# Kernel optimization log

Hardware: AMD Instinct MI355X
Metric: run time of the kernel (lower is better)

## Reference

```python
import jax, jax.numpy as jnp
import numpy as np
import math

N_NODES = 100000
N_EDGES = 3200000

_SQRT3 = math.sqrt(3.0)
_SQRT5 = math.sqrt(5.0)


def _spherical_harmonics_lmax2(v):
    """e3nn real spherical harmonics, lmax=2, normalize=True, normalization='component'.

    v: [E, 3] edge vectors (not necessarily unit).
    Returns [E, 9] = concat(Y0 [1], Y1 [3], Y2 [5]).
    """
    # normalize=True: evaluate SH on the unit vector
    u = v / jnp.linalg.norm(v, axis=1, keepdims=True)
    x, y, z = u[:, 0], u[:, 1], u[:, 2]
    # l=0 (component norm: *sqrt(1) = 1)
    sh0 = jnp.ones_like(x)
    # l=1 (component norm: *sqrt(3))
    sh1_0 = _SQRT3 * x
    sh1_1 = _SQRT3 * y
    sh1_2 = _SQRT3 * z
    # l=2 raw polynomials (norm-1 at unit vector), then *sqrt(5) for component norm
    x2, y2, z2 = x * x, y * y, z * z
    sh2_0 = _SQRT3 * x * z
    sh2_1 = _SQRT3 * x * y
    sh2_2 = y2 - 0.5 * (x2 + z2)
    sh2_3 = _SQRT3 * y * z
    sh2_4 = 0.5 * _SQRT3 * (z2 - x2)
    sh2 = _SQRT5 * jnp.stack([sh2_0, sh2_1, sh2_2, sh2_3, sh2_4], axis=-1)
    return jnp.concatenate(
        [sh0[:, None], jnp.stack([sh1_0, sh1_1, sh1_2], axis=-1), sh2], axis=-1
    )


def setup_inputs() -> dict:
    key = jax.random.key(0)
    k1, k2, k3 = jax.random.split(key, 3)
    pos = jax.random.normal(k1, (N_NODES, 3), dtype=jnp.float32)
    edge_index = jax.random.randint(k2, (2, N_EDGES), 0, N_NODES, dtype=jnp.int64)
    shift = jax.random.normal(k3, (N_EDGES, 3), dtype=jnp.float32)
    return {"pos": pos, "edge_index": edge_index, "shift": shift}


def reference(pos, edge_index, shift):
    # gather endpoints and form displacement vectors
    edge_vec = pos[edge_index[1]] - pos[edge_index[0]]  # [E, 3]
    edge_vec = edge_vec - shift
    edge_length = jnp.linalg.norm(edge_vec, axis=1)  # [E]
    edge_sh = _spherical_harmonics_lmax2(edge_vec)  # [E, 9]
    return (edge_vec, edge_length, edge_sh)
```

## Files before the change

### kernel.cpp

```cpp
#include <hip/hip_runtime.h>
#include <math.h>


#define SQRT3 1.7320508075688772f
#define SQRT5 2.2360679774997896f

typedef float v4f __attribute__((ext_vector_type(4)));

__global__ __launch_bounds__(256) void sh_edge_kernel(
    const float*  __restrict__ pos,
    const int*    __restrict__ edge_index,
    const float*  __restrict__ shift,
    float* __restrict__ out_vec,
    float* __restrict__ out_len,
    float* __restrict__ out_sh,
    int n_edges)
{
    __shared__ float s_shift[768];
    __shared__ float s_vec[768];
    __shared__ float s_sh[2304];

    const int tid  = threadIdx.x;
    const int base = blockIdx.x * 256;
    const int nblk = min(256, n_edges - base);
    const bool full = (nblk == 256);

    float psx = 0.f, psy = 0.f, psz = 0.f, pdx = 0.f, pdy = 0.f, pdz = 0.f;
    if (tid < nblk) {
        const int e = base + tid;
        const int s = __builtin_nontemporal_load(&edge_index[e]);
        const int d = __builtin_nontemporal_load(&edge_index[n_edges + e]);
        const float* ps = pos + 3 * (size_t)s;
        const float* pd = pos + 3 * (size_t)d;
        psx = ps[0]; psy = ps[1]; psz = ps[2];
        pdx = pd[0]; pdy = pd[1]; pdz = pd[2];
    }

    if (full) {
        const v4f* g = reinterpret_cast<const v4f*>(shift + 3 * (size_t)base);
        if (tid < 192) {
            v4f v = __builtin_nontemporal_load(&g[tid]);
            reinterpret_cast<v4f*>(s_shift)[tid] = v;
        }
    } else {
        for (int i = tid; i < 3 * nblk; i += 256)
            s_shift[i] = shift[3 * (size_t)base + i];
    }
    __syncthreads();

    if (tid < nblk) {
        const int e = base + tid;

        float x = pdx - psx - s_shift[3 * tid + 0];
        float y = pdy - psy - s_shift[3 * tid + 1];
        float z = pdz - psz - s_shift[3 * tid + 2];

        s_vec[3 * tid + 0] = x;
        s_vec[3 * tid + 1] = y;
        s_vec[3 * tid + 2] = z;

        float sq = x * x + y * y + z * z;
        float r  = rsqrtf(sq);
        __builtin_nontemporal_store(sq * r, &out_len[e]);

        float nx = x * r, ny = y * r, nz = z * r;
        float x2 = nx * nx, y2 = ny * ny, z2 = nz * nz;

        float* o = s_sh + 9 * tid;
        o[0] = 1.0f;
        o[1] = SQRT3 * nx;
        o[2] = SQRT3 * ny;
        o[3] = SQRT3 * nz;
        o[4] = SQRT5 * SQRT3 * nx * nz;
        o[5] = SQRT5 * SQRT3 * nx * ny;
        o[6] = SQRT5 * (y2 - 0.5f * (x2 + z2));
        o[7] = SQRT5 * SQRT3 * ny * nz;
        o[8] = SQRT5 * 0.5f * SQRT3 * (z2 - x2);
    }
    __syncthreads();

    if (full) {
        v4f* gv = reinterpret_cast<v4f*>(out_vec + 3 * (size_t)base);
        const v4f* lv = reinterpret_cast<const v4f*>(s_vec);
        if (tid < 192) __builtin_nontemporal_store(lv[tid], &gv[tid]);

        v4f* gs = reinterpret_cast<v4f*>(out_sh + 9 * (size_t)base);
        const v4f* ls = reinterpret_cast<const v4f*>(s_sh);
        __builtin_nontemporal_store(ls[tid],       &gs[tid]);
        __builtin_nontemporal_store(ls[256 + tid], &gs[256 + tid]);
        if (tid < 64) __builtin_nontemporal_store(ls[512 + tid], &gs[512 + tid]);
    } else {
        for (int i = tid; i < 3 * nblk; i += 256) out_vec[3 * (size_t)base + i] = s_vec[i];
        for (int i = tid; i < 9 * nblk; i += 256) out_sh[9 * (size_t)base + i]  = s_sh[i];
    }
}

extern "C" void kernel_launch(void* const* d_in, const int* in_sizes, int n_in,
                              void* d_out, int out_size, void* d_ws, size_t ws_size,
                              hipStream_t stream) {
    const float* pos        = (const float*)d_in[0];
    const int*   edge_index = (const int*)d_in[1];
    const float* shift      = (const float*)d_in[2];

    const int n_edges = in_sizes[2] / 3;

    float* out_vec = (float*)d_out;
    float* out_len = (float*)d_out + 3 * (size_t)n_edges;
    float* out_sh  = (float*)d_out + 4 * (size_t)n_edges;

    const int blocks = (n_edges + 255) / 256;
    sh_edge_kernel<<<blocks, 256, 0, stream>>>(
        pos, edge_index, shift, out_vec, out_len, out_sh, n_edges);
}
```

Before: 246.8 us.

## Drop LDS staging and write outputs directly per thread

Removes the shared-memory staging of shift, edge vectors and spherical harmonics, along with both block barriers. Each thread now loads its own shift triple and writes its 3 vector floats and 9 SH floats straight to global memory with strided scalar accesses. This trades the vectorized, fully coalesced 16-byte stores for uncoalesced strided scalar stores, relying on the caches and write combining to merge them. It removes LDS traffic and synchronization overhead.

After: 271.4 us. 10.0% more time.

```diff
diff --git a/kernel.cpp b/kernel.cpp
--- a/kernel.cpp
+++ b/kernel.cpp
@@ -4,8 +4,6 @@
 
 #define SQRT3 1.7320508075688772f
 #define SQRT5 2.2360679774997896f
-
-typedef float v4f __attribute__((ext_vector_type(4)));
 
 __global__ __launch_bounds__(256) void sh_edge_kernel(
     const float*  __restrict__ pos,
@@ -16,83 +14,48 @@
     float* __restrict__ out_sh,
     int n_edges)
 {
-    __shared__ float s_shift[768];
-    __shared__ float s_vec[768];
-    __shared__ float s_sh[2304];
+    const int e = blockIdx.x * 256 + threadIdx.x;
+    if (e >= n_edges) return;
 
-    const int tid  = threadIdx.x;
-    const int base = blockIdx.x * 256;
-    const int nblk = min(256, n_edges - base);
-    const bool full = (nblk == 256);
+    const int s = __builtin_nontemporal_load(&edge_index[e]);
+    const int d = __builtin_nontemporal_load(&edge_index[n_edges + e]);
 
-    float psx = 0.f, psy = 0.f, psz = 0.f, pdx = 0.f, pdy = 0.f, pdz = 0.f;
-    if (tid < nblk) {
-        const int e = base + tid;
-        const int s = __builtin_nontemporal_load(&edge_index[e]);
-        const int d = __builtin_nontemporal_load(&edge_index[n_edges + e]);
-        const float* ps = pos + 3 * (size_t)s;
-        const float* pd = pos + 3 * (size_t)d;
-        psx = ps[0]; psy = ps[1]; psz = ps[2];
-        pdx = pd[0]; pdy = pd[1]; pdz = pd[2];
+    const float* sp = shift + 3 * (size_t)e;
+    const float shx = sp[0], shy = sp[1], shz = sp[2];
+
+    const float* ps = pos + 3 * (size_t)s;
+    const float* pd = pos + 3 * (size_t)d;
+    const float ax = ps[0], ay = ps[1], az = ps[2];
+    const float bx = pd[0], by = pd[1], bz = pd[2];
+
+    const float x = bx - ax - shx;
+    const float y = by - ay - shy;
+    const float z = bz - az - shz;
+
+    {
+        float* ov = out_vec + 3 * (size_t)e;
+        __builtin_nontemporal_store(x, &ov[0]);
+        __builtin_nontemporal_store(y, &ov[1]);
+        __builtin_nontemporal_store(z, &ov[2]);
     }
 
-    if (full) {
-        const v4f* g = reinterpret_cast<const v4f*>(shift + 3 * (size_t)base);
-        if (tid < 192) {
-            v4f v = __builtin_nontemporal_load(&g[tid]);
-            reinterpret_cast<v4f*>(s_shift)[tid] = v;
-        }
-    } else {
-        for (int i = tid; i < 3 * nblk; i += 256)
-            s_shift[i] = shift[3 * (size_t)base + i];
-    }
-    __syncthreads();
+    const float sq = x * x + y * y + z * z;
+    const float r  = rsqrtf(sq);
+    __builtin_nontemporal_store(sq * r, &out_len[e]);
 
-    if (tid < nblk) {
-        const int e = base + tid;
+    const float nx = x * r, ny = y * r, nz = z * r;
+    const float x2 = nx * nx, y2 = ny * ny, z2 = nz * nz;
 
-        float x = pdx - psx - s_shift[3 * tid + 0];
-        float y = pdy - psy - s_shift[3 * tid + 1];
-        float z = pdz - psz - s_shift[3 * tid + 2];
-
-        s_vec[3 * tid + 0] = x;
-        s_vec[3 * tid + 1] = y;
-        s_vec[3 * tid + 2] = z;
-
-        float sq = x * x + y * y + z * z;
-        float r  = rsqrtf(sq);
-        __builtin_nontemporal_store(sq * r, &out_len[e]);
-
-        float nx = x * r, ny = y * r, nz = z * r;
-        float x2 = nx * nx, y2 = ny * ny, z2 = nz * nz;
-
-        float* o = s_sh + 9 * tid;
-        o[0] = 1.0f;
-        o[1] = SQRT3 * nx;
-        o[2] = SQRT3 * ny;
-        o[3] = SQRT3 * nz;
-        o[4] = SQRT5 * SQRT3 * nx * nz;
-        o[5] = SQRT5 * SQRT3 * nx * ny;
-        o[6] = SQRT5 * (y2 - 0.5f * (x2 + z2));
-        o[7] = SQRT5 * SQRT3 * ny * nz;
-        o[8] = SQRT5 * 0.5f * SQRT3 * (z2 - x2);
-    }
-    __syncthreads();
-
-    if (full) {
-        v4f* gv = reinterpret_cast<v4f*>(out_vec + 3 * (size_t)base);
-        const v4f* lv = reinterpret_cast<const v4f*>(s_vec);
-        if (tid < 192) __builtin_nontemporal_store(lv[tid], &gv[tid]);
-
-        v4f* gs = reinterpret_cast<v4f*>(out_sh + 9 * (size_t)base);
-        const v4f* ls = reinterpret_cast<const v4f*>(s_sh);
-        __builtin_nontemporal_store(ls[tid],       &gs[tid]);
-        __builtin_nontemporal_store(ls[256 + tid], &gs[256 + tid]);
-        if (tid < 64) __builtin_nontemporal_store(ls[512 + tid], &gs[512 + tid]);
-    } else {
-        for (int i = tid; i < 3 * nblk; i += 256) out_vec[3 * (size_t)base + i] = s_vec[i];
-        for (int i = tid; i < 9 * nblk; i += 256) out_sh[9 * (size_t)base + i]  = s_sh[i];
-    }
+    float* o = out_sh + 9 * (size_t)e;
+    o[0] = 1.0f;
+    o[1] = SQRT3 * nx;
+    o[2] = SQRT3 * ny;
+    o[3] = SQRT3 * nz;
+    o[4] = SQRT5 * SQRT3 * nx * nz;
+    o[5] = SQRT5 * SQRT3 * nx * ny;
+    o[6] = SQRT5 * (y2 - 0.5f * (x2 + z2));
+    o[7] = SQRT5 * SQRT3 * ny * nz;
+    o[8] = SQRT5 * 0.5f * SQRT3 * (z2 - x2);
 }
 
 extern "C" void kernel_launch(void* const* d_in, const int* in_sizes, int n_in,
```
